# Kernel tuning notes

Measured on AMD Instinct MI355X. Metric: run time of the kernel, lower is better.

## Reference

```python
import jax, jax.numpy as jnp
import numpy as np

B, T, D, A = 8, 256, 512, 512  # hidden dim D must equal attn size A per the TF code


def setup_inputs() -> dict:
    key = jax.random.key(0)
    ks = jax.random.split(key, 12)
    g = lambda k, shp, fan: jax.random.normal(k, shp, jnp.float32) * (1.0 / np.sqrt(fan))
    return {
        "state_outputs": jax.random.normal(ks[0], (B, T, D), jnp.float32),
        "final_state": jax.random.normal(ks[1], (B, D), jnp.float32),
        "intent_v": g(ks[2], (A,), A),
        "W_ih": g(ks[3], (D, A), D), "b_ih": jnp.zeros((A,), jnp.float32),
        "W_ii": g(ks[4], (D, A), D), "b_ii": jnp.zeros((A,), jnp.float32),
        "slot_v": g(ks[5], (A,), A),
        "W_sh": g(ks[6], (D, A), D), "b_sh": jnp.zeros((A,), jnp.float32),
        "W_si": g(ks[7], (D, A), D), "b_si": jnp.zeros((A,), jnp.float32),
    }


def reference(state_outputs, final_state, intent_v, W_ih, b_ih, W_ii, b_ii,
              slot_v, W_sh, b_sh, W_si, b_si):
    # ---- intent attention ----
    ih = jnp.einsum('btd,da->bta', state_outputs, W_ih) + b_ih        # [B,T,A]
    ii = final_state @ W_ii + b_ii                                     # [B,A]
    intent_score = jnp.sum(intent_v * jnp.tanh(ih + ii[:, None, :]), axis=-1)  # [B,T]
    intent_w = jax.nn.softmax(intent_score, axis=-1)
    c_intent = jnp.einsum('bt,btd->bd', intent_w, state_outputs)       # [B,D]

    # ---- slot attention ----
    sh = jnp.einsum('btd,da->bta', state_outputs, W_sh) + b_sh         # keys   [B,T,A]
    si = jnp.einsum('btd,da->bta', state_outputs, W_si) + b_si         # queries[B,T,A]
    # score[b,t,s] over pairs: tanh(sh[b,s] + si[b,t]) . slot_v
    slot_score = jnp.sum(slot_v * jnp.tanh(sh[:, None, :, :] + si[:, :, None, :]), axis=-1)  # [B,T,T]
    slot_w = jax.nn.softmax(slot_score, axis=-1)
    c_slot = jnp.einsum('bts,bsd->btd', slot_w, state_outputs)         # [B,T,D]
    return c_slot, c_intent
```

## Files before the change

kernel.cpp:

```cpp
#include <hip/hip_runtime.h>

#define BB 8
#define TT 256
#define DD 512
#define AA 512

#define PS 2.8853900817779268f
#define LOG2E 1.4426950408889634f

typedef __attribute__((ext_vector_type(8))) short short8;
typedef __attribute__((ext_vector_type(4))) float f32x4;

__device__ __forceinline__ float fast_tanh(float x) {
    float e = __builtin_amdgcn_exp2f(x * PS);
    float r = __builtin_amdgcn_rcpf(1.0f + e);
    return fmaf(-2.0f, r, 1.0f);
}

__device__ __forceinline__ ushort f2bf(float x) {
    uint u = __float_as_uint(x);
    uint r = (u + 0x7fffu + ((u >> 16) & 1u)) >> 16;
    return (ushort)r;
}
__device__ __forceinline__ float bf2f(ushort h) {
    return __uint_as_float(((uint)h) << 16);
}

__global__ __launch_bounds__(256) void prep(const float* __restrict__ SO,
                                            ushort* __restrict__ Ast,
                                            const float* __restrict__ Wsh,
                                            const float* __restrict__ Wsi,
                                            const float* __restrict__ Wih,
                                            ushort* __restrict__ Wt,
                                            const float* __restrict__ fs_g,
                                            const float* __restrict__ Wii,
                                            const float* __restrict__ bii,
                                            float* __restrict__ ii) {
    const int bid = blockIdx.x;
    const int tid = threadIdx.x;
    __shared__ float T[32][33];
    __shared__ float fs[DD];

    if (bid < 1024) {
        int qid = bid * 256 + tid;
        int m = qid >> 7;
        int k4 = (qid & 127) * 4;
        float4 v = *reinterpret_cast<const float4*>(&SO[(size_t)m * 512 + k4]);
        ushort4 hi, lo;
        hi.x = f2bf(v.x); lo.x = f2bf(v.x - bf2f(hi.x));
        hi.y = f2bf(v.y); lo.y = f2bf(v.y - bf2f(hi.y));
        hi.z = f2bf(v.z); lo.z = f2bf(v.z - bf2f(hi.z));
        hi.w = f2bf(v.w); lo.w = f2bf(v.w - bf2f(hi.w));
        *reinterpret_cast<ushort4*>(&Ast[(size_t)m * 1024 + k4])       = hi;
        *reinterpret_cast<ushort4*>(&Ast[(size_t)m * 1024 + 512 + k4]) = lo;
    } else if (bid < 1792) {
        int lbid = bid - 1024;
        int z = lbid >> 8;
        int rem = lbid & 255;
        const float* W = (z == 0) ? Wsh : (z == 1) ? Wsi : Wih;
        int k0 = (rem & 15) * 32, n0 = (rem >> 4) * 32;
        int tx = tid & 31, ty = tid >> 5;
        #pragma unroll
        for (int r = 0; r < 4; ++r) {
            int kl = ty * 4 + r;
            T[kl][tx] = W[(size_t)(k0 + kl) * 512 + n0 + tx];
        }
        __syncthreads();
        size_t nbase = (size_t)z * 512 + n0;
        #pragma unroll
        for (int r = 0; r < 4; ++r) {
            int nl = ty * 4 + r;
            float v = T[tx][nl];
            ushort hi = f2bf(v);
            ushort lo = f2bf(v - bf2f(hi));
            Wt[(nbase + nl) * 1024 + k0 + tx]       = hi;
            Wt[(nbase + nl) * 1024 + 512 + k0 + tx] = lo;
        }
    } else {
        int lbid = bid - 1792;
        int b = lbid >> 1, half = lbid & 1;
        int a = half * 256 + tid;
        fs[tid]       = fs_g[b * DD + tid];
        fs[tid + 256] = fs_g[b * DD + tid + 256];
        __syncthreads();
        float acc = bii[a];
        #pragma unroll 8
        for (int d = 0; d < DD; ++d)
            acc = fmaf(fs[d], Wii[(size_t)d * AA + a], acc);
        ii[b * AA + a] = acc;
    }
}

__global__ __launch_bounds__(256) void gemm_mfma(
    const ushort* __restrict__ Ast, const ushort* __restrict__ Wt,
    const float* __restrict__ bsh, const float* __restrict__ bsi,
    const float* __restrict__ bih,
    const float* __restrict__ ii, const float* __restrict__ iv,
    float* __restrict__ EhT, float* __restrict__ Es, float* __restrict__ ipart) {
    __shared__ ushort Al[64 * 64];
    __shared__ ushort Bl[64 * 64];
    const int tid = threadIdx.x;
    const int wave = tid >> 6, lane = tid & 63;
    const int wr = wave >> 1, wc = wave & 1;
    const int m0 = blockIdx.x * 64;
    const int by = blockIdx.y;
    const int n0 = by * 64;
    const int r8 = lane >> 3, c8 = lane & 7;
    const int l15 = lane & 15, kb = lane >> 4;

    f32x4 acc[2][2] = {};

    const char* Ab = reinterpret_cast<const char*>(Ast);
    const char* Bb = reinterpret_cast<const char*>(Wt);
    char* AlB = reinterpret_cast<char*>(Al);
    char* BlB = reinterpret_cast<char*>(Bl);

    for (int k0 = 0; k0 < 1536; k0 += 64) {
        int abyte = (k0 < 1024 ? k0 : k0 - 1024) * 2;
        int bbyte = (k0 < 512 ? k0 : k0 - 512) * 2;
        #pragma unroll
        for (int inst = 0; inst < 2; ++inst) {
            int row = wave * 16 + inst * 8 + r8;
            short8 av = *reinterpret_cast<const short8*>(
                Ab + (size_t)(m0 + row) * 2048 + abyte + c8 * 16);
            *reinterpret_cast<short8*>(AlB + row * 128 + ((c8 ^ r8) * 16)) = av;
            short8 bv = *reinterpret_cast<const short8*>(
                Bb + (size_t)(n0 + row) * 2048 + bbyte + c8 * 16);
            *reinterpret_cast<short8*>(BlB + row * 128 + ((c8 ^ r8) * 16)) = bv;
        }
        __syncthreads();
        #pragma unroll
        for (int kk = 0; kk < 2; ++kk) {
            short8 af[2], bf[2];
            #pragma unroll
            for (int i = 0; i < 2; ++i) {
                int ra = wr * 32 + i * 16 + l15;
                int sa = (kk * 4 + kb) ^ (ra & 7);
                af[i] = *reinterpret_cast<const short8*>(AlB + ra * 128 + sa * 16);
                int rb = wc * 32 + i * 16 + l15;
                int sbx = (kk * 4 + kb) ^ (rb & 7);
                bf[i] = *reinterpret_cast<const short8*>(BlB + rb * 128 + sbx * 16);
            }
            #pragma unroll
            for (int i = 0; i < 2; ++i)
                #pragma unroll
                for (int j = 0; j < 2; ++j)
                    acc[i][j] = __builtin_amdgcn_mfma_f32_16x16x32_bf16(
                        af[i], bf[j], acc[i][j], 0, 0, 0);
        }
        __syncthreads();
    }

    const int b = m0 >> 8;
    if (by < 8) {
        #pragma unroll
        for (int i = 0; i < 2; ++i) {
            int t0 = (m0 & 255) + wr * 32 + i * 16 + kb * 4;
            #pragma unroll
            for (int j = 0; j < 2; ++j) {
                int n = n0 + wc * 32 + j * 16 + l15;
                float bbv = bsh[n];
                float4 v;
                v.x = __builtin_amdgcn_exp2f((acc[i][j][0] + bbv) * PS);
                v.y = __builtin_amdgcn_exp2f((acc[i][j][1] + bbv) * PS);
                v.z = __builtin_amdgcn_exp2f((acc[i][j][2] + bbv) * PS);
                v.w = __builtin_amdgcn_exp2f((acc[i][j][3] + bbv) * PS);
                *reinterpret_cast<float4*>(&EhT[((size_t)b * 512 + n) * 256 + t0]) = v;
            }
        }
    } else if (by < 16) {
        #pragma unroll
        for (int i = 0; i < 2; ++i) {
            #pragma unroll
            for (int j = 0; j < 2; ++j) {
                int n = n0 - 512 + wc * 32 + j * 16 + l15;
                float bbv = bsi[n];
                #pragma unroll
                for (int r = 0; r < 4; ++r) {
                    int m = m0 + wr * 32 + i * 16 + kb * 4 + r;
                    Es[(size_t)m * 512 + n] = __builtin_amdgcn_exp2f((acc[i][j][r] + bbv) * PS);
                }
            }
        }
    } else {
        int slot = (by - 16) * 2 + wc;
        #pragma unroll
        for (int i = 0; i < 2; ++i) {
            float p0 = 0.f, p1 = 0.f, p2 = 0.f, p3 = 0.f;
            #pragma unroll
            for (int j = 0; j < 2; ++j) {
                int n = n0 - 1024 + wc * 32 + j * 16 + l15;
                float add = bih[n] + ii[b * 512 + n];
                float w = iv[n];
                p0 = fmaf(w, fast_tanh(acc[i][j][0] + add), p0);
                p1 = fmaf(w, fast_tanh(acc[i][j][1] + add), p1);
                p2 = fmaf(w, fast_tanh(acc[i][j][2] + add), p2);
                p3 = fmaf(w, fast_tanh(acc[i][j][3] + add), p3);
            }
            #pragma unroll
            for (int off = 1; off < 16; off <<= 1) {
                p0 += __shfl_xor(p0, off);
                p1 += __shfl_xor(p1, off);
                p2 += __shfl_xor(p2, off);
                p3 += __shfl_xor(p3, off);
            }
            int mb = m0 + wr * 32 + i * 16 + kb * 4;
            if (l15 == 0) ipart[slot * 2048 + mb + 0] = p0;
            if (l15 == 1) ipart[slot * 2048 + mb + 1] = p1;
            if (l15 == 2) ipart[slot * 2048 + mb + 2] = p2;
            if (l15 == 3) ipart[slot * 2048 + mb + 3] = p3;
        }
    }
}

#define TS 64
#define KS 16
#define LPAD 72

__global__ __launch_bounds__(256) void k0_ii(const float* __restrict__ fs_g,
                                             const float* __restrict__ Wii,
                                             const float* __restrict__ bii,
                                             float* __restrict__ ii) {
    int b = blockIdx.x, tid = threadIdx.x;
    int a = blockIdx.y * 256 + tid;
    __shared__ float fs[DD];
    fs[tid]       = fs_g[b * DD + tid];
    fs[tid + 256] = fs_g[b * DD + tid + 256];
    __syncthreads();
    float acc = bii[a];
    #pragma unroll 8
    for (int d = 0; d < DD; ++d)
        acc = fmaf(fs[d], Wii[(size_t)d * AA + a], acc);
    ii[b * AA + a] = acc;
}

__global__ __launch_bounds__(256) void k1_gemm_old(
    const float* __restrict__ SO,
    const float* __restrict__ Wsh, const float* __restrict__ bsh,
    const float* __restrict__ Wsi, const float* __restrict__ bsi,
    const float* __restrict__ Wih, const float* __restrict__ bih,
    const float* __restrict__ ii, const float* __restrict__ iv,
    float* __restrict__ EhT, float* __restrict__ Es, float* __restrict__ ipart) {
    const int mode = blockIdx.z;
    const float* W;
    const float* bias;
    if (mode == 0)      { W = Wsh; bias = bsh; }
    else if (mode == 1) { W = Wsi; bias = bsi; }
    else                { W = Wih; bias = bih; }

    const int m0 = blockIdx.x * TS;
    const int n0 = blockIdx.y * TS;
    const int tid = threadIdx.x;
    const int tx = tid & 15, ty = tid >> 4;

    __shared__ __align__(16) float As[KS][LPAD];
    __shared__ __align__(16) float Bs[KS][LPAD];
    __shared__ __align__(16) float Cs[TS][LPAD];

    float acc[4][4] = {};
    const int arow = tid >> 2;
    const int akc  = (tid & 3) * 4;
    const int brw  = tid >> 4;
    const int bnc  = (tid & 15) * 4;

    for (int k0 = 0; k0 < DD; k0 += KS) {
        float4 av = *reinterpret_cast<const float4*>(&SO[(m0 + arow) * DD + k0 + akc]);
        As[akc + 0][arow] = av.x;
        As[akc + 1][arow] = av.y;
        As[akc + 2][arow] = av.z;
        As[akc + 3][arow] = av.w;
        float4 bv = *reinterpret_cast<const float4*>(&W[(k0 + brw) * AA + n0 + bnc]);
        *reinterpret_cast<float4*>(&Bs[brw][bnc]) = bv;
        __syncthreads();
        #pragma unroll
        for (int kk = 0; kk < KS; ++kk) {
            float4 a4 = *reinterpret_cast<const float4*>(&As[kk][ty * 4]);
            float4 b4 = *reinterpret_cast<const float4*>(&Bs[kk][tx * 4]);
            float av_[4] = {a4.x, a4.y, a4.z, a4.w};
            float bv_[4] = {b4.x, b4.y, b4.z, b4.w};
            #pragma unroll
            for (int i = 0; i < 4; ++i)
                #pragma unroll
                for (int j = 0; j < 4; ++j)
                    acc[i][j] = fmaf(av_[i], bv_[j], acc[i][j]);
        }
        __syncthreads();
    }

    if (mode == 1) {
        #pragma unroll
        for (int i = 0; i < 4; ++i) {
            int m = m0 + ty * 4 + i;
            float4 v;
            v.x = __builtin_amdgcn_exp2f((acc[i][0] + bias[n0 + tx * 4 + 0]) * PS);
            v.y = __builtin_amdgcn_exp2f((acc[i][1] + bias[n0 + tx * 4 + 1]) * PS);
            v.z = __builtin_amdgcn_exp2f((acc[i][2] + bias[n0 + tx * 4 + 2]) * PS);
            v.w = __builtin_amdgcn_exp2f((acc[i][3] + bias[n0 + tx * 4 + 3]) * PS);
            *reinterpret_cast<float4*>(&Es[(size_t)m * AA + n0 + tx * 4]) = v;
        }
    } else if (mode == 0) {
        #pragma unroll
        for (int i = 0; i < 4; ++i)
            #pragma unroll
            for (int j = 0; j < 4; ++j)
                Cs[tx * 4 + j][ty * 4 + i] =
                    __builtin_amdgcn_exp2f((acc[i][j] + bias[n0 + tx * 4 + j]) * PS);
        __syncthreads();
        int row = tid >> 2, part = tid & 3;
        int bb = m0 >> 8;
        int tstart = (m0 & 255) + part * 16;
        float* dst = &EhT[bb * (AA * TT) + (n0 + row) * TT + tstart];
        #pragma unroll
        for (int q = 0; q < 4; ++q) {
            float4 v = *reinterpret_cast<const float4*>(&Cs[row][part * 16 + q * 4]);
            *reinterpret_cast<float4*>(&dst[q * 4]) = v;
        }
    } else {
        int bb = m0 >> 8;
        #pragma unroll
        for (int i = 0; i < 4; ++i) {
            float p = 0.f;
            #pragma unroll
            for (int j = 0; j < 4; ++j) {
                int n = n0 + tx * 4 + j;
                float x = acc[i][j] + bias[n] + ii[bb * AA + n];
                p = fmaf(iv[n], fast_tanh(x), p);
            }
            Cs[ty * 4 + i][tx] = p;
        }
        __syncthreads();
        if (tid < 64) {
            float s = 0.f;
            #pragma unroll
            for (int k = 0; k < 16; ++k) s += Cs[tid][k];
            ipart[blockIdx.y * 2048 + m0 + tid] = s;
        }
    }
}

__global__ __launch_bounds__(512) void k3_fused(const float* __restrict__ SO,
                                                const float* __restrict__ EhT,
                                                const float* __restrict__ Es,
                                                const float* __restrict__ sv_g,
                                                const float* __restrict__ ipart,
                                                float* __restrict__ out_cslot,
                                                float* __restrict__ out_cint,
                                                int npart) {
    const int bid = blockIdx.x;
    const int tid = threadIdx.x;

    __shared__ __align__(16) float est[512][4];
    __shared__ float sv[512];
    __shared__ float yp[2][4][256];
    __shared__ __align__(16) float wlt[256][4];
    __shared__ float redm[4][4];
    __shared__ float reds[4][4];
    __shared__ float redI[256];
    __shared__ float wlI[256];

    if (bid < 512) {
        const int b = bid & 7;
        const int t0 = (bid >> 3) * 4;
        const int s = tid & 255, ah = tid >> 8;

        {
            const float* esrc = &Es[(size_t)(b * 256 + t0) * 512];
            #pragma unroll
            for (int i = tid; i < 2048; i += 512) est[i & 511][i >> 9] = esrc[i];
            sv[tid] = sv_g[tid];
        }
        __syncthreads();

        const int abase = ah * 256;
        const float* hp = &EhT[((size_t)b * 512 + abase) * 256 + s];
        float y0 = 0.f, y1 = 0.f, y2 = 0.f, y3 = 0.f;
        for (int a0 = 0; a0 < 256; a0 += 8) {
            float h[8];
            #pragma unroll
            for (int u = 0; u < 8; ++u) h[u] = hp[(a0 + u) * 256];
            #pragma unroll
            for (int u = 0; u < 8; ++u) {
                int a = abase + a0 + u;
                float4 e4 = *reinterpret_cast<const float4*>(&est[a][0]);
                float v = sv[a];
                float x0 = fmaf(h[u], e4.x, 1.0f);
                y0 = fmaf(v, __builtin_amdgcn_rcpf(x0), y0);
                float x1 = fmaf(h[u], e4.y, 1.0f);
                y1 = fmaf(v, __builtin_amdgcn_rcpf(x1), y1);
                float x2 = fmaf(h[u], e4.z, 1.0f);
                y2 = fmaf(v, __builtin_amdgcn_rcpf(x2), y2);
                float x3 = fmaf(h[u], e4.w, 1.0f);
                y3 = fmaf(v, __builtin_amdgcn_rcpf(x3), y3);
            }
        }
        yp[ah][0][s] = y0; yp[ah][1][s] = y1; yp[ah][2][s] = y2; yp[ah][3][s] = y3;
        __syncthreads();

        const int wg = (tid >> 6) & 3;
        #pragma unroll
        for (int r = 0; r < 2; ++r) {
            int q = ah * 2 + r;
            float y = yp[0][q][s] + yp[1][q][s];
            float mn = y;
            #pragma unroll
            for (int off = 1; off < 64; off <<= 1)
                mn = fminf(mn, __shfl_xor(mn, off));
            if ((tid & 63) == 0) redm[q][wg] = mn;
            __syncthreads();
            mn = fminf(fminf(redm[q][0], redm[q][1]), fminf(redm[q][2], redm[q][3]));
            float e = __builtin_amdgcn_exp2f(PS * (mn - y));
            float sm = e;
            #pragma unroll
            for (int off = 1; off < 64; off <<= 1)
                sm += __shfl_xor(sm, off);
            if ((tid & 63) == 0) reds[q][wg] = sm;
            __syncthreads();
            sm = (reds[q][0] + reds[q][1]) + (reds[q][2] + reds[q][3]);
            wlt[s][q] = e * __builtin_amdgcn_rcpf(sm);
        }
        __syncthreads();

        const int d = tid;
        const float* sop = &SO[(size_t)b * 256 * 512 + d];
        float c0 = 0.f, c1 = 0.f, c2 = 0.f, c3 = 0.f;
        for (int s0 = 0; s0 < 256; s0 += 4) {
            float so[4];
            #pragma unroll
            for (int u = 0; u < 4; ++u) so[u] = sop[(s0 + u) * 512];
            #pragma unroll
            for (int u = 0; u < 4; ++u) {
                float4 w4 = *reinterpret_cast<const float4*>(&wlt[s0 + u][0]);
                c0 = fmaf(w4.x, so[u], c0);
                c1 = fmaf(w4.y, so[u], c1);
                c2 = fmaf(w4.z, so[u], c2);
                c3 = fmaf(w4.w, so[u], c3);
            }
        }
        float* op = &out_cslot[((size_t)(b * 256 + t0)) * 512 + d];
        op[0] = c0; op[512] = c1; op[1024] = c2; op[1536] = c3;
    } else {
        const int b = bid - 512;
        float sc = 0.f;
        if (tid < 256) {
            for (int nb = 0; nb < npart; ++nb) sc += ipart[nb * 2048 + b * 256 + tid];
            redI[tid] = sc;
        }
        __syncthreads();
        for (int off = 128; off > 0; off >>= 1) {
            if (tid < off) redI[tid] = fmaxf(redI[tid], redI[tid + off]);
            __syncthreads();
        }
        float mx = redI[0];
        __syncthreads();
        float e = 0.f;
        if (tid < 256) { e = __builtin_amdgcn_exp2f((sc - mx) * LOG2E); redI[tid] = e; }
        __syncthreads();
        for (int off = 128; off > 0; off >>= 1) {
            if (tid < off) redI[tid] += redI[tid + off];
            __syncthreads();
        }
        if (tid < 256) wlI[tid] = e * __builtin_amdgcn_rcpf(redI[0]);
        __syncthreads();
        const int d = tid;
        float c = 0.f;
        const float* sop = &SO[(size_t)b * 256 * 512 + d];
        for (int s0 = 0; s0 < 256; s0 += 4) {
            float so[4];
            #pragma unroll
            for (int u = 0; u < 4; ++u) so[u] = sop[(s0 + u) * 512];
            #pragma unroll
            for (int u = 0; u < 4; ++u) c = fmaf(wlI[s0 + u], so[u], c);
        }
        out_cint[(size_t)b * 512 + d] = c;
    }
}

extern "C" void kernel_launch(void* const* d_in, const int* in_sizes, int n_in,
                              void* d_out, int out_size, void* d_ws, size_t ws_size,
                              hipStream_t stream) {
    const float* SO  = (const float*)d_in[0];
    const float* FS  = (const float*)d_in[1];
    const float* IV  = (const float*)d_in[2];
    const float* Wih = (const float*)d_in[3];
    const float* bih = (const float*)d_in[4];
    const float* Wii = (const float*)d_in[5];
    const float* bii = (const float*)d_in[6];
    const float* SV  = (const float*)d_in[7];
    const float* Wsh = (const float*)d_in[8];
    const float* bsh = (const float*)d_in[9];
    const float* Wsi = (const float*)d_in[10];
    const float* bsi = (const float*)d_in[11];

    float* ws    = (float*)d_ws;
    float* EhT   = ws;
    float* Es    = ws + 1048576;
    float* ii    = ws + 2097152;
    float* ipart = ws + 2101248;
    ushort* Ast  = (ushort*)(ws + 2134016);
    ushort* Wt   = (ushort*)(ws + 3182592);
    const size_t NEED = (size_t)3969024 * 4;

    float* out_cslot = (float*)d_out;
    float* out_cint  = out_cslot + BB * TT * DD;

    if (ws_size >= NEED) {
        prep<<<1808, 256, 0, stream>>>(SO, Ast, Wsh, Wsi, Wih, Wt, FS, Wii, bii, ii);
        gemm_mfma<<<dim3(32, 24), 256, 0, stream>>>(Ast, Wt, bsh, bsi, bih, ii, IV,
                                                    EhT, Es, ipart);
        k3_fused<<<520, 512, 0, stream>>>(SO, EhT, Es, SV, ipart, out_cslot, out_cint, 16);
    } else {
        k0_ii<<<dim3(BB, 2), 256, 0, stream>>>(FS, Wii, bii, ii);
        k1_gemm_old<<<dim3(32, 8, 3), 256, 0, stream>>>(SO, Wsh, bsh, Wsi, bsi, Wih, bih,
                                                        ii, IV, EhT, Es, ipart);
        k3_fused<<<520, 512, 0, stream>>>(SO, EhT, Es, SV, ipart, out_cslot, out_cint, 8);
    }
}
```

Measured before the change: 107.4 us.

## Load MFMA fragments directly from global with 3-stage register pipeline

The bf16 split GEMM no longer stages A/B tiles through shared memory with barriers. Each wave loads its own MFMA fragments straight from global memory into registers, using a triple-buffered register prefetch so loads overlap with the MFMAs. The prep and final kernels also reorder their block roles so the short ii and intent blocks are scheduled first. Without LDS, each tile is fetched from global or L2 once per wave rather than shared across the block, and register use goes up.

```diff
diff --git a/kernel.cpp b/kernel.cpp
--- a/kernel.cpp
+++ b/kernel.cpp
@@ -41,8 +41,42 @@
     __shared__ float T[32][33];
     __shared__ float fs[DD];
 
-    if (bid < 1024) {
-        int qid = bid * 256 + tid;
+    if (bid < 16) {
+        int b = bid >> 1, half = bid & 1;
+        int a = half * 256 + tid;
+        fs[tid]       = fs_g[b * DD + tid];
+        fs[tid + 256] = fs_g[b * DD + tid + 256];
+        __syncthreads();
+        float acc = bii[a];
+        #pragma unroll 8
+        for (int d = 0; d < DD; ++d)
+            acc = fmaf(fs[d], Wii[(size_t)d * AA + a], acc);
+        ii[b * AA + a] = acc;
+    } else if (bid < 784) {
+        int lbid = bid - 16;
+        int z = lbid >> 8;
+        int rem = lbid & 255;
+        const float* W = (z == 0) ? Wsh : (z == 1) ? Wsi : Wih;
+        int k0 = (rem & 15) * 32, n0 = (rem >> 4) * 32;
+        int tx = tid & 31, ty = tid >> 5;
+        #pragma unroll
+        for (int r = 0; r < 4; ++r) {
+            int kl = ty * 4 + r;
+            T[kl][tx] = W[(size_t)(k0 + kl) * 512 + n0 + tx];
+        }
+        __syncthreads();
+        size_t nbase = (size_t)z * 512 + n0;
+        #pragma unroll
+        for (int r = 0; r < 4; ++r) {
+            int nl = ty * 4 + r;
+            float v = T[tx][nl];
+            ushort hi = f2bf(v);
+            ushort lo = f2bf(v - bf2f(hi));
+            Wt[(nbase + nl) * 1024 + k0 + tx]       = hi;
+            Wt[(nbase + nl) * 1024 + 512 + k0 + tx] = lo;
+        }
+    } else {
+        int qid = (bid - 784) * 256 + tid;
         int m = qid >> 7;
         int k4 = (qid & 127) * 4;
         float4 v = *reinterpret_cast<const float4*>(&SO[(size_t)m * 512 + k4]);
@@ -53,41 +87,6 @@
         hi.w = f2bf(v.w); lo.w = f2bf(v.w - bf2f(hi.w));
         *reinterpret_cast<ushort4*>(&Ast[(size_t)m * 1024 + k4])       = hi;
         *reinterpret_cast<ushort4*>(&Ast[(size_t)m * 1024 + 512 + k4]) = lo;
-    } else if (bid < 1792) {
-        int lbid = bid - 1024;
-        int z = lbid >> 8;
-        int rem = lbid & 255;
-        const float* W = (z == 0) ? Wsh : (z == 1) ? Wsi : Wih;
-        int k0 = (rem & 15) * 32, n0 = (rem >> 4) * 32;
-        int tx = tid & 31, ty = tid >> 5;
-        #pragma unroll
-        for (int r = 0; r < 4; ++r) {
-            int kl = ty * 4 + r;
-            T[kl][tx] = W[(size_t)(k0 + kl) * 512 + n0 + tx];
-        }
-        __syncthreads();
-        size_t nbase = (size_t)z * 512 + n0;
-        #pragma unroll
-        for (int r = 0; r < 4; ++r) {
-            int nl = ty * 4 + r;
-            float v = T[tx][nl];
-            ushort hi = f2bf(v);
-            ushort lo = f2bf(v - bf2f(hi));
-            Wt[(nbase + nl) * 1024 + k0 + tx]       = hi;
-            Wt[(nbase + nl) * 1024 + 512 + k0 + tx] = lo;
-        }
-    } else {
-        int lbid = bid - 1792;
-        int b = lbid >> 1, half = lbid & 1;
-        int a = half * 256 + tid;
-        fs[tid]       = fs_g[b * DD + tid];
-        fs[tid + 256] = fs_g[b * DD + tid + 256];
-        __syncthreads();
-        float acc = bii[a];
-        #pragma unroll 8
-        for (int d = 0; d < DD; ++d)
-            acc = fmaf(fs[d], Wii[(size_t)d * AA + a], acc);
-        ii[b * AA + a] = acc;
     }
 }
 
@@ -97,58 +96,51 @@
     const float* __restrict__ bih,
     const float* __restrict__ ii, const float* __restrict__ iv,
     float* __restrict__ EhT, float* __restrict__ Es, float* __restrict__ ipart) {
-    __shared__ ushort Al[64 * 64];
-    __shared__ ushort Bl[64 * 64];
     const int tid = threadIdx.x;
     const int wave = tid >> 6, lane = tid & 63;
     const int wr = wave >> 1, wc = wave & 1;
     const int m0 = blockIdx.x * 64;
     const int by = blockIdx.y;
     const int n0 = by * 64;
-    const int r8 = lane >> 3, c8 = lane & 7;
     const int l15 = lane & 15, kb = lane >> 4;
 
     f32x4 acc[2][2] = {};
 
-    const char* Ab = reinterpret_cast<const char*>(Ast);
-    const char* Bb = reinterpret_cast<const char*>(Wt);
-    char* AlB = reinterpret_cast<char*>(Al);
-    char* BlB = reinterpret_cast<char*>(Bl);
-
-    for (int k0 = 0; k0 < 1536; k0 += 64) {
-        int abyte = (k0 < 1024 ? k0 : k0 - 1024) * 2;
-        int bbyte = (k0 < 512 ? k0 : k0 - 512) * 2;
-        #pragma unroll
-        for (int inst = 0; inst < 2; ++inst) {
-            int row = wave * 16 + inst * 8 + r8;
-            short8 av = *reinterpret_cast<const short8*>(
-                Ab + (size_t)(m0 + row) * 2048 + abyte + c8 * 16);
-            *reinterpret_cast<short8*>(AlB + row * 128 + ((c8 ^ r8) * 16)) = av;
-            short8 bv = *reinterpret_cast<const short8*>(
-                Bb + (size_t)(n0 + row) * 2048 + bbyte + c8 * 16);
-            *reinterpret_cast<short8*>(BlB + row * 128 + ((c8 ^ r8) * 16)) = bv;
-        }
-        __syncthreads();
-        #pragma unroll
-        for (int kk = 0; kk < 2; ++kk) {
-            short8 af[2], bf[2];
-            #pragma unroll
-            for (int i = 0; i < 2; ++i) {
-                int ra = wr * 32 + i * 16 + l15;
-                int sa = (kk * 4 + kb) ^ (ra & 7);
-                af[i] = *reinterpret_cast<const short8*>(AlB + ra * 128 + sa * 16);
-                int rb = wc * 32 + i * 16 + l15;
-                int sbx = (kk * 4 + kb) ^ (rb & 7);
-                bf[i] = *reinterpret_cast<const short8*>(BlB + rb * 128 + sbx * 16);
-            }
-            #pragma unroll
-            for (int i = 0; i < 2; ++i)
-                #pragma unroll
-                for (int j = 0; j < 2; ++j)
-                    acc[i][j] = __builtin_amdgcn_mfma_f32_16x16x32_bf16(
-                        af[i], bf[j], acc[i][j], 0, 0, 0);
-        }
-        __syncthreads();
+    const char* Arow0 = reinterpret_cast<const char*>(Ast)
+                        + (size_t)(m0 + wr * 32 + l15) * 2048 + kb * 16;
+    const char* Arow1 = Arow0 + 16 * 2048;
+    const char* Brow0 = reinterpret_cast<const char*>(Wt)
+                        + (size_t)(n0 + wc * 32 + l15) * 2048 + kb * 16;
+    const char* Brow1 = Brow0 + 16 * 2048;
+
+    #define GLOAD(AF, BF, S) do {                                                  \
+        const int kl_ = (S) * 32;                                                  \
+        const int ab_ = (kl_ < 1024 ? kl_ : kl_ - 1024) * 2;                       \
+        const int bb_ = (kl_ < 512  ? kl_ : kl_ - 512 ) * 2;                       \
+        AF[0] = *reinterpret_cast<const short8*>(Arow0 + ab_);                     \
+        AF[1] = *reinterpret_cast<const short8*>(Arow1 + ab_);                     \
+        BF[0] = *reinterpret_cast<const short8*>(Brow0 + bb_);                     \
+        BF[1] = *reinterpret_cast<const short8*>(Brow1 + bb_);                     \
+    } while (0)
+
+    #define DOMFMA(AF, BF) do {                                                    \
+        acc[0][0] = __builtin_amdgcn_mfma_f32_16x16x32_bf16(AF[0], BF[0], acc[0][0], 0, 0, 0); \
+        acc[0][1] = __builtin_amdgcn_mfma_f32_16x16x32_bf16(AF[0], BF[1], acc[0][1], 0, 0, 0); \
+        acc[1][0] = __builtin_amdgcn_mfma_f32_16x16x32_bf16(AF[1], BF[0], acc[1][0], 0, 0, 0); \
+        acc[1][1] = __builtin_amdgcn_mfma_f32_16x16x32_bf16(AF[1], BF[1], acc[1][1], 0, 0, 0); \
+    } while (0)
+
+    short8 f0A[2], f0B[2], f1A[2], f1B[2], f2A[2], f2B[2];
+    GLOAD(f0A, f0B, 0);
+    GLOAD(f1A, f1B, 1);
+    for (int it = 0; it < 16; ++it) {
+        const int s = it * 3;
+        GLOAD(f2A, f2B, s + 2);
+        DOMFMA(f0A, f0B);
+        if (s + 3 < 48) GLOAD(f0A, f0B, s + 3);
+        DOMFMA(f1A, f1B);
+        if (s + 4 < 48) GLOAD(f1A, f1B, s + 4);
+        DOMFMA(f2A, f2B);
     }
 
     const int b = m0 >> 8;
@@ -358,9 +350,10 @@
     __shared__ float redI[256];
     __shared__ float wlI[256];
 
-    if (bid < 512) {
-        const int b = bid & 7;
-        const int t0 = (bid >> 3) * 4;
+    if (bid >= 8) {
+        const int sb_ = bid - 8;
+        const int b = sb_ & 7;
+        const int t0 = (sb_ >> 3) * 4;
         const int s = tid & 255, ah = tid >> 8;
 
         {
@@ -439,7 +432,7 @@
         float* op = &out_cslot[((size_t)(b * 256 + t0)) * 512 + d];
         op[0] = c0; op[512] = c1; op[1024] = c2; op[1536] = c3;
     } else {
-        const int b = bid - 512;
+        const int b = bid;
         float sc = 0.f;
         if (tid < 256) {
             for (int nb = 0; nb < npart; ++nb) sc += ipart[nb * 2048 + b * 256 + tid];
```

Result: slower. 129.0 us (+20.0%).
